# Kernel optimization log

Measured on AMD Instinct MI355X. Metric: run time of the kernel, lower is better.

## Reference

```python
import jax, jax.numpy as jnp
import numpy as np

N, E, B, H, L = 100000, 200000, 2048, 256, 4
EPS_MSG = 1e-7   # GENConv message eps
LN_EPS = 1e-5    # torch LayerNorm default eps
SM_EPS = 1e-16   # PyG softmax denominator eps


def layer_norm(x, g, b):
    mu = x.mean(-1, keepdims=True)
    var = ((x - mu) ** 2).mean(-1, keepdims=True)
    return (x - mu) * jax.lax.rsqrt(var + LN_EPS) * g + b


def gen_conv(x, src, dst, eattr, t, W1, b1, lg, lb, W2, b2):
    # GENConv(aggr='softmax', learn_t, num_layers=2, norm='layer')
    msg = jax.nn.relu(x[src] + eattr) + EPS_MSG                      # [E,H]
    scaled = msg * t
    seg_max = jax.ops.segment_max(scaled, dst, num_segments=N)       # [N,H]
    seg_max = jnp.where(jnp.isfinite(seg_max), seg_max, 0.0)
    ex = jnp.exp(scaled - seg_max[dst])                              # [E,H]
    denom = jax.ops.segment_sum(ex, dst, num_segments=N)             # [N,H]
    alpha = ex / (denom[dst] + SM_EPS)
    out = jax.ops.segment_sum(msg * alpha, dst, num_segments=N)      # [N,H]
    out = out + x                                                    # root residual inside GENConv
    h = jax.nn.relu(layer_norm(out @ W1 + b1, lg, lb))               # MLP: Lin -> LN -> ReLU -> Lin
    return h @ W2 + b2


def setup_inputs() -> dict:
    key = jax.random.key(0)
    ks = iter(jax.random.split(key, 16))
    s = lambda *sh: jax.random.normal(next(ks), sh, jnp.float32) * 0.05
    return dict(
        x=jax.random.normal(next(ks), (N, 9), jnp.float32),
        edge_index=jax.random.randint(next(ks), (2, E), 0, N),
        edge_attr=jax.random.normal(next(ks), (E, 3), jnp.float32),
        batch=jnp.sort(jax.random.randint(next(ks), (N,), 0, B)),
        node_W=s(9, H), node_b=jnp.zeros((H,), jnp.float32),
        edge_W=s(3, H), edge_b=jnp.zeros((H,), jnp.float32),
        vn_emb=jnp.zeros((1, H), jnp.float32),
        ln_g=jnp.ones((L, H), jnp.float32), ln_b=jnp.zeros((L, H), jnp.float32),
        t=jnp.ones((L - 1,), jnp.float32),
        mlp_W1=s(L - 1, H, 2 * H), mlp_b1=jnp.zeros((L - 1, 2 * H), jnp.float32),
        mlp_ln_g=jnp.ones((L - 1, 2 * H), jnp.float32), mlp_ln_b=jnp.zeros((L - 1, 2 * H), jnp.float32),
        mlp_W2=s(L - 1, 2 * H, H), mlp_b2=jnp.zeros((L - 1, H), jnp.float32),
    )


def reference(x, edge_index, edge_attr, batch, node_W, node_b, edge_W, edge_b,
              vn_emb, ln_g, ln_b, t, mlp_W1, mlp_b1, mlp_ln_g, mlp_ln_b, mlp_W2, mlp_b2):
    src, dst = edge_index[0], edge_index[1]
    h = x @ node_W + node_b                                          # node encoder
    ea = edge_attr @ edge_W + edge_b                                 # edge encoder
    vn = jnp.broadcast_to(vn_emb, (B, H))
    counts = jax.ops.segment_sum(jnp.ones((N,), h.dtype), batch, num_segments=B)
    inv_counts = (1.0 / jnp.maximum(counts, 1.0))[:, None]           # [B,1]
    # layers[1:] run conv (block='res+'); layers[0] supplies only the final norm+act
    for l in range(1, L):
        hn = jax.nn.relu(layer_norm(h, ln_g[l], ln_b[l]))            # dropout=0.1 is a no-op in eval
        h = h + gen_conv(hn, src, dst, ea, t[l - 1],
                         mlp_W1[l - 1], mlp_b1[l - 1], mlp_ln_g[l - 1], mlp_ln_b[l - 1],
                         mlp_W2[l - 1], mlp_b2[l - 1])
        vn = vn + jax.ops.segment_sum(h, batch, num_segments=B) * inv_counts  # scatter_mean
        h = h + vn[batch]                                            # broadcast virtual node
    h = jax.nn.relu(layer_norm(h, ln_g[0], ln_b[0]))
    return jax.ops.segment_sum(h, batch, num_segments=B) * inv_counts  # global_mean_pool [B,H]
```

## Files before the change

### kernel.cpp

```cpp
#include <hip/hip_runtime.h>
#include <cstdint>
#include <cstddef>


typedef _Float16 half8_t __attribute__((ext_vector_type(8)));
typedef _Float16 half4_t __attribute__((ext_vector_type(4)));
typedef float    floatx4 __attribute__((ext_vector_type(4)));

#define DEVINL __device__ __forceinline__

DEVINL float wave_sum(float v) {
#pragma unroll
  for (int m = 32; m; m >>= 1) v += __shfl_xor(v, m, 64);
  return v;
}

__global__ __launch_bounds__(256) void k_node_enc(
    const float* __restrict__ x, const float* __restrict__ W,
    const float* __restrict__ bias, _Float16* __restrict__ h, int Nr) {
  __shared__ float sW[9 * 256];
  __shared__ float sb[256];
  __shared__ float sx[72];
  const int j = threadIdx.x;
#pragma unroll
  for (int k = 0; k < 9; ++k) sW[k * 256 + j] = W[k * 256 + j];
  sb[j] = bias[j];
  const int row0 = blockIdx.x * 8;
  if (j < 72) {
    int p = row0 * 9 + j;
    sx[j] = (p < Nr * 9) ? x[p] : 0.f;
  }
  __syncthreads();
  for (int r = 0; r < 8; ++r) {
    int row = row0 + r;
    if (row >= Nr) break;
    float acc = sb[j];
#pragma unroll
    for (int k = 0; k < 9; ++k) acc = fmaf(sx[r * 9 + k], sW[k * 256 + j], acc);
    h[(size_t)row * 256 + j] = (_Float16)acc;
  }
}

__global__ void k_bptr(const int* __restrict__ batch, int* __restrict__ bptr,
                       int N_, int B_) {
  int b = blockIdx.x * 256 + threadIdx.x;
  if (b > B_) return;
  int lo = 0, hi = N_;
  while (lo < hi) {
    int mid = (lo + hi) >> 1;
    if (batch[mid] < b) lo = mid + 1; else hi = mid;
  }
  bptr[b] = lo;
}

__global__ void k_deg(const int* __restrict__ ei, int* __restrict__ deg, int E_) {
  int e = blockIdx.x * 256 + threadIdx.x;
  if (e < E_) atomicAdd(&deg[ei[E_ + e]], 1);
}

__global__ __launch_bounds__(256) void k_scan1(
    const int* __restrict__ in, int* __restrict__ out1, int* __restrict__ bsum, int n) {
  __shared__ int tmp[256];
  const int t = threadIdx.x;
  const int base = blockIdx.x * 1024;
  int v[4];
  int run = 0;
#pragma unroll
  for (int i = 0; i < 4; ++i) {
    int p = base + t * 4 + i;
    int xv = (p < n) ? in[p] : 0;
    run += xv;
    v[i] = run;
  }
  tmp[t] = run;
  __syncthreads();
  for (int off = 1; off < 256; off <<= 1) {
    int u = (t >= off) ? tmp[t - off] : 0;
    __syncthreads();
    tmp[t] += u;
    __syncthreads();
  }
  int excl = tmp[t] - run;
#pragma unroll
  for (int i = 0; i < 4; ++i) {
    int p = base + t * 4 + i;
    if (p < n) out1[p] = v[i] + excl;
  }
  if (t == 255) bsum[blockIdx.x] = tmp[255];
}

__global__ void k_scan2(int* bsum, int nb, int* ptr0) {
  if (threadIdx.x == 0 && blockIdx.x == 0) {
    int run = 0;
    for (int i = 0; i < nb; ++i) { int xv = bsum[i]; bsum[i] = run; run += xv; }
    ptr0[0] = 0;
  }
}

__global__ __launch_bounds__(256) void k_scan3(int* out1, const int* __restrict__ bsum, int n) {
  int add = bsum[blockIdx.x];
  int p0 = blockIdx.x * 1024 + threadIdx.x * 4;
#pragma unroll
  for (int i = 0; i < 4; ++i) {
    int p = p0 + i;
    if (p < n) out1[p] += add;
  }
}

__global__ void k_copy(const int* __restrict__ a, int* __restrict__ b, int n) {
  int i = blockIdx.x * 256 + threadIdx.x;
  if (i < n) b[i] = a[i];
}

__global__ void k_csrfill(const int* __restrict__ ei, int* __restrict__ cursor,
                          int* __restrict__ csr_src, int* __restrict__ csr_eid, int E_) {
  int e = blockIdx.x * 256 + threadIdx.x;
  if (e < E_) {
    int d = ei[E_ + e];
    int pos = atomicAdd(&cursor[d], 1);
    csr_src[pos] = ei[e];
    csr_eid[pos] = e;
  }
}

__global__ void k_vninit(const float* __restrict__ emb, float* __restrict__ vn) {
  vn[(size_t)blockIdx.x * 256 + threadIdx.x] = emb[threadIdx.x];
}

__global__ __launch_bounds__(256) void k_wcvt_all(
    const float* __restrict__ W1, const float* __restrict__ W2,
    _Float16* __restrict__ W1T, _Float16* __restrict__ W2T) {
  int idx = blockIdx.x * 256 + threadIdx.x;
  int mat = idx >> 17;
  int rem = idx & 131071;
  if (mat < 3) {
    int k = rem >> 9, n = rem & 511;
    W1T[(size_t)mat * 131072 + (size_t)n * 256 + k] =
        (_Float16)W1[(size_t)mat * 131072 + rem];
  } else {
    int m = mat - 3;
    int k = rem >> 8, n = rem & 255;
    W2T[(size_t)m * 131072 + (size_t)n * 512 + k] =
        (_Float16)W2[(size_t)m * 131072 + rem];
  }
}

template <int VN>
__global__ __launch_bounds__(256) void k_ln256(
    const _Float16* __restrict__ h, const float* __restrict__ vn,
    const int* __restrict__ batch, const float* __restrict__ g,
    const float* __restrict__ b, _Float16* __restrict__ out, int Nr) {
  int row = blockIdx.x * 4 + (threadIdx.x >> 6);
  if (row >= Nr) return;
  int lane = threadIdx.x & 63;
  half4_t xh = *(const half4_t*)(h + (size_t)row * 256 + lane * 4);
  float4 xv = {(float)xh[0], (float)xh[1], (float)xh[2], (float)xh[3]};
  if constexpr (VN) {
    int bb = batch[row];
    float4 vv = *(const float4*)(vn + (size_t)bb * 256 + lane * 4);
    xv.x += vv.x; xv.y += vv.y; xv.z += vv.z; xv.w += vv.w;
  }
  float s = wave_sum(xv.x + xv.y + xv.z + xv.w);
  float mu = s * (1.f / 256.f);
  float d0 = xv.x - mu, d1 = xv.y - mu, d2 = xv.z - mu, d3 = xv.w - mu;
  float v = wave_sum(d0 * d0 + d1 * d1 + d2 * d2 + d3 * d3);
  float rstd = rsqrtf(v * (1.f / 256.f) + 1e-5f);
  float4 gv = *(const float4*)(g + lane * 4);
  float4 bv = *(const float4*)(b + lane * 4);
  half4_t o;
  o[0] = (_Float16)fmaxf(d0 * rstd * gv.x + bv.x, 0.f);
  o[1] = (_Float16)fmaxf(d1 * rstd * gv.y + bv.y, 0.f);
  o[2] = (_Float16)fmaxf(d2 * rstd * gv.z + bv.z, 0.f);
  o[3] = (_Float16)fmaxf(d3 * rstd * gv.w + bv.w, 0.f);
  *(half4_t*)(out + (size_t)row * 256 + lane * 4) = o;
}

__global__ __launch_bounds__(256) void k_aggregate(
    const _Float16* __restrict__ hn, const float* __restrict__ eattr,
    const float* __restrict__ edgeW, const float* __restrict__ edgeB,
    const int* __restrict__ indptr, const int* __restrict__ csr_src,
    const int* __restrict__ csr_eid, const float* __restrict__ tptr,
    _Float16* __restrict__ agg, int Nr) {
  __shared__ float sW[4 * 256];
  const int tj = threadIdx.x;
  sW[tj] = edgeW[tj];
  sW[256 + tj] = edgeW[256 + tj];
  sW[512 + tj] = edgeW[512 + tj];
  sW[768 + tj] = edgeB[tj];
  __syncthreads();

  int node = blockIdx.x * 4 + (threadIdx.x >> 6);
  if (node >= Nr) return;
  int lane = threadIdx.x & 63;
  float tval = tptr[0];
  int e0 = indptr[node], e1 = indptr[node + 1];
  float M[4], D[4], Nu[4];
#pragma unroll
  for (int i = 0; i < 4; ++i) { M[i] = -1e38f; D[i] = 0.f; Nu[i] = 0.f; }
  for (int s = e0; s < e1; ++s) {
    int srcn = csr_src[s];
    int eid = csr_eid[s];
    float ex0 = eattr[(size_t)eid * 3 + 0];
    float ex1 = eattr[(size_t)eid * 3 + 1];
    float ex2 = eattr[(size_t)eid * 3 + 2];
    half4_t hv = *(const half4_t*)(hn + (size_t)srcn * 256 + lane * 4);
#pragma unroll
    for (int i = 0; i < 4; ++i) {
      int j = lane * 4 + i;
      float eaj = fmaf(ex0, sW[j], fmaf(ex1, sW[256 + j], fmaf(ex2, sW[512 + j], sW[768 + j])));
      float msg = fmaxf((float)hv[i] + eaj, 0.f) + 1e-7f;
      float sc = msg * tval;
      float nM = fmaxf(M[i], sc);
      float sOld = __expf(M[i] - nM);
      float pr = __expf(sc - nM);
      D[i] = D[i] * sOld + pr;
      Nu[i] = Nu[i] * sOld + pr * msg;
      M[i] = nM;
    }
  }
  half4_t hs = *(const half4_t*)(hn + (size_t)node * 256 + lane * 4);
  half4_t res;
#pragma unroll
  for (int i = 0; i < 4; ++i)
    res[i] = (_Float16)(Nu[i] / (D[i] + 1e-16f) + (float)hs[i]);
  *(half4_t*)(agg + (size_t)node * 256 + lane * 4) = res;
}

__global__ __launch_bounds__(256, 2) void k_gemm1(
    const _Float16* __restrict__ A, const _Float16* __restrict__ BT,
    const float* __restrict__ bias, _Float16* __restrict__ outh,
    float2* __restrict__ rstat, int M) {
  __shared__ _Float16 ldsA[128 * 256];
  __shared__ _Float16 ldsB[128 * 64];
  const int tid = threadIdx.x;
  const int lane = tid & 63;
  const int wv = tid >> 6;
  const int m0 = blockIdx.x * 128;
  const int wm = wv * 32;
  const int q = lane >> 4;
  const int l16 = lane & 15;

  for (int g = 0; g < 4; ++g) {
    half8_t tmp[4];
    int ss[4];
#pragma unroll
    for (int i = 0; i < 4; ++i) {
      int s = (g * 4 + i) * 256 + tid;
      int r = s >> 5;
      int c = (s & 31) ^ (r & 7);
      int rowA = m0 + r;
      rowA = rowA < M ? rowA : (M - 1);
      tmp[i] = *(const half8_t*)(A + (size_t)rowA * 256 + c * 8);
      ss[i] = s;
    }
#pragma unroll
    for (int i = 0; i < 4; ++i)
      *(half8_t*)(ldsA + (size_t)ss[i] * 8) = tmp[i];
  }

  size_t offB[4];
  int ldsOffB[4];
#pragma unroll
  for (int i = 0; i < 4; ++i) {
    int p = (i * 4 + wv) * 64 + lane;
    int r = p >> 3;
    int s = p & 7;
    int gg = s ^ (r & 7);
    offB[i] = (size_t)r * 256 + gg * 8;
    ldsOffB[i] = p * 8;
  }
  half8_t rb[4];
  auto loadB = [&](int j) {
    int n = j >> 2, t = j & 3;
    size_t base = (size_t)n * 128 * 256 + t * 64;
#pragma unroll
    for (int i = 0; i < 4; ++i)
      rb[i] = *(const half8_t*)(BT + base + offB[i]);
  };
  auto writeB = [&]() {
#pragma unroll
    for (int i = 0; i < 4; ++i)
      *(half8_t*)(ldsB + ldsOffB[i]) = rb[i];
  };

  floatx4 acc[2][8] = {};
  float sA[2][4] = {}, s2A[2][4] = {};

  loadB(0);
  writeB();
  for (int j = 0; j < 16; ++j) {
    __syncthreads();
    if (j + 1 < 16) loadB(j + 1);
    const int t = j & 3;
#pragma unroll
    for (int kk = 0; kk < 2; ++kk) {
      const int c8 = kk * 4 + q;
      const int cg = t * 8 + c8;
      half8_t af[2], bf[8];
#pragma unroll
      for (int rt = 0; rt < 2; ++rt) {
        int r = wm + rt * 16 + l16;
        af[rt] = *(const half8_t*)(ldsA + (size_t)(r * 32 + (cg ^ (r & 7))) * 8);
      }
#pragma unroll
      for (int ct = 0; ct < 8; ++ct) {
        int n = ct * 16 + l16;
        bf[ct] = *(const half8_t*)(ldsB + (size_t)(n * 8 + (c8 ^ (n & 7))) * 8);
      }
#pragma unroll
      for (int rt = 0; rt < 2; ++rt)
#pragma unroll
        for (int ct = 0; ct < 8; ++ct)
          acc[rt][ct] = __builtin_amdgcn_mfma_f32_16x16x32_f16(af[rt], bf[ct], acc[rt][ct], 0, 0, 0);
    }
    __syncthreads();
    if (j + 1 < 16) writeB();
    if ((j & 3) == 3) {
      int n = j >> 2;
#pragma unroll
      for (int rt = 0; rt < 2; ++rt) {
#pragma unroll
        for (int rr = 0; rr < 4; ++rr) {
          int row = m0 + wm + rt * 16 + q * 4 + rr;
          float vv[8];
          float s = 0.f, s2 = 0.f;
#pragma unroll
          for (int ct = 0; ct < 8; ++ct) {
            int col = n * 128 + ct * 16 + l16;
            float v = acc[rt][ct][rr] + bias[col];
            vv[ct] = v;
            s += v;
            s2 += v * v;
          }
          if (row < M) {
#pragma unroll
            for (int ct = 0; ct < 8; ++ct) {
              int col = n * 128 + ct * 16 + l16;
              outh[(size_t)row * 512 + col] = (_Float16)vv[ct];
            }
          }
          sA[rt][rr] += s;
          s2A[rt][rr] += s2;
        }
      }
#pragma unroll
      for (int rt = 0; rt < 2; ++rt)
#pragma unroll
        for (int ct = 0; ct < 8; ++ct)
          acc[rt][ct] = floatx4{0.f, 0.f, 0.f, 0.f};
    }
  }

#pragma unroll
  for (int rt = 0; rt < 2; ++rt) {
#pragma unroll
    for (int rr = 0; rr < 4; ++rr) {
      float s = sA[rt][rr], s2 = s2A[rt][rr];
#pragma unroll
      for (int m = 1; m < 16; m <<= 1) {
        s += __shfl_xor(s, m, 64);
        s2 += __shfl_xor(s2, m, 64);
      }
      int row = m0 + wm + rt * 16 + q * 4 + rr;
      if (l16 == 0 && row < M) rstat[row] = make_float2(s, s2);
    }
  }
}

template <int VN>
__global__ __launch_bounds__(256, 2) void k_gemm2(
    const _Float16* __restrict__ A, const _Float16* __restrict__ BT,
    const float* __restrict__ bias, const float2* __restrict__ rstat,
    const float* __restrict__ lg, const float* __restrict__ lb,
    const float* __restrict__ vn, const int* __restrict__ batch,
    _Float16* __restrict__ outf, int M) {
  constexpr int K = 512, NN = 256, NT = K / 64;
  constexpr int EPS = 68;
  const int g = blockIdx.x;
  const int mI = blockIdx.y * 8 + (g & 7);
  const int nI = g >> 3;
  const int mT = (M + 127) >> 7;
  if (mI >= mT) return;

  __shared__ _Float16 ldsbuf[4 * 64 * EPS];
  _Float16* ldsA = ldsbuf;
  _Float16* ldsB = ldsbuf + 128 * 64;
  __shared__ float sg[512];
  __shared__ float sbt[512];
  const int tid = threadIdx.x;
  sg[tid] = lg[tid];
  sg[tid + 256] = lg[tid + 256];
  sbt[tid] = lb[tid];
  sbt[tid + 256] = lb[tid + 256];
  __syncthreads();

  const int lane = tid & 63;
  const int wv = tid >> 6;
  const int m0 = mI * 128;
  const int n0 = nI * 128;
  const int wm = (wv >> 1) * 64;
  const int wn = (wv & 1) * 64;
  const int q = lane >> 4;
  const int l16 = lane & 15;
  floatx4 acc[4][4] = {};

  size_t offA[4], offB[4];
  int ldsOff[4], gcolA[4];
  float aco[4], cco[4];
#pragma unroll
  for (int i = 0; i < 4; ++i) {
    int p = (i * 4 + wv) * 64 + lane;
    int r = p >> 3;
    int s = p & 7;
    int gg = s ^ (r & 7);
    int rowA = m0 + r;
    rowA = rowA < M ? rowA : (M - 1);
    offA[i] = (size_t)rowA * K + gg * 8;
    offB[i] = (size_t)(n0 + r) * K + gg * 8;
    ldsOff[i] = p * 8;
    gcolA[i] = gg * 8;
    float2 st = rstat[rowA];
    float mu = st.x * (1.f / 512.f);
    float var = st.y * (1.f / 512.f) - mu * mu;
    float rs = rsqrtf(var + 1e-5f);
    aco[i] = rs;
    cco[i] = -mu * rs;
  }
  half8_t ra[4], rb[4];
  auto loadtile = [&](int kt) {
#pragma unroll
    for (int i = 0; i < 4; ++i) {
      ra[i] = *(const half8_t*)(A + offA[i] + kt);
      rb[i] = *(const half8_t*)(BT + offB[i] + kt);
    }
  };
  auto writetile = [&](int kt) {
#pragma unroll
    for (int i = 0; i < 4; ++i) {
      int c0 = kt + gcolA[i];
      half8_t ya;
#pragma unroll
      for (int jj = 0; jj < 8; ++jj) {
        float e = fmaf((float)ra[i][jj], aco[i], cco[i]);
        float y = fmaf(e, sg[c0 + jj], sbt[c0 + jj]);
        ya[jj] = (_Float16)fmaxf(y, 0.f);
      }
      *(half8_t*)(ldsA + ldsOff[i]) = ya;
      *(half8_t*)(ldsB + ldsOff[i]) = rb[i];
    }
  };

  loadtile(0);
  writetile(0);
#pragma unroll
  for (int t = 0; t < NT; ++t) {
    __syncthreads();
    if (t + 1 < NT) loadtile((t + 1) * 64);
#pragma unroll
    for (int kk = 0; kk < 2; ++kk) {
      half8_t af[4], bf[4];
      const int c8 = kk * 4 + q;
#pragma unroll
      for (int rt = 0; rt < 4; ++rt) {
        int r = wm + rt * 16 + l16;
        af[rt] = *(const half8_t*)(ldsA + (size_t)(r * 8 + (c8 ^ (r & 7))) * 8);
      }
#pragma unroll
      for (int ct = 0; ct < 4; ++ct) {
        int n = wn + ct * 16 + l16;
        bf[ct] = *(const half8_t*)(ldsB + (size_t)(n * 8 + (c8 ^ (n & 7))) * 8);
      }
#pragma unroll
      for (int rt = 0; rt < 4; ++rt)
#pragma unroll
        for (int ct = 0; ct < 4; ++ct)
          acc[rt][ct] = __builtin_amdgcn_mfma_f32_16x16x32_f16(af[rt], bf[ct], acc[rt][ct], 0, 0, 0);
    }
    __syncthreads();
    if (t + 1 < NT) writetile((t + 1) * 64);
  }

  _Float16* epi = ldsbuf + wv * (64 * EPS);
#pragma unroll
  for (int rt = 0; rt < 4; ++rt) {
#pragma unroll
    for (int rr = 0; rr < 4; ++rr) {
      int rloc = rt * 16 + q * 4 + rr;
      int row = m0 + wm + rloc;
      int rowc = row < M ? row : (M - 1);
      int bb = 0;
      if constexpr (VN) bb = batch[rowc];
#pragma unroll
      for (int ct = 0; ct < 4; ++ct) {
        int cloc = ct * 16 + l16;
        int col = n0 + wn + cloc;
        float v = acc[rt][ct][rr] + bias[col];
        if constexpr (VN) v += vn[(size_t)bb * 256 + col];
        epi[rloc * EPS + cloc] = (_Float16)v;
      }
    }
  }
#pragma unroll
  for (int it = 0; it < 8; ++it) {
    int rloc = it * 8 + (lane >> 3);
    int row = m0 + wm + rloc;
    if (row < M) {
      int c0 = (lane & 7) * 8;
      size_t gidx = (size_t)row * NN + n0 + wn + c0;
      half8_t hv = *(const half8_t*)(outf + gidx);
      half8_t ev = *(const half8_t*)(epi + rloc * EPS + c0);
      half8_t o;
#pragma unroll
      for (int jj = 0; jj < 8; ++jj) o[jj] = (_Float16)((float)hv[jj] + (float)ev[jj]);
      *(half8_t*)(outf + gidx) = o;
    }
  }
}

__global__ __launch_bounds__(256) void k_vnsum(
    const _Float16* __restrict__ h, float* __restrict__ vn,
    const int* __restrict__ bptr) {
  int b = blockIdx.x, j = threadIdx.x;
  int n0 = bptr[b], n1 = bptr[b + 1];
  float acc = 0.f;
  for (int n = n0; n < n1; ++n) acc += (float)h[(size_t)n * 256 + j];
  int c = n1 - n0;
  vn[(size_t)b * 256 + j] += acc * (1.f / (float)(c > 1 ? c : 1));
}

__global__ __launch_bounds__(256) void k_lnpool(
    const _Float16* __restrict__ h, const float* __restrict__ vn,
    const int* __restrict__ bptr, const float* __restrict__ g,
    const float* __restrict__ b, float* __restrict__ out) {
  __shared__ float red[3][256];
  int bb = blockIdx.x;
  int w = threadIdx.x >> 6;
  int lane = threadIdx.x & 63;
  int n0 = bptr[bb], n1 = bptr[bb + 1];
  float4 vv = *(const float4*)(vn + (size_t)bb * 256 + lane * 4);
  float4 gv = *(const float4*)(g + lane * 4);
  float4 bv = *(const float4*)(b + lane * 4);
  float a0 = 0.f, a1 = 0.f, a2 = 0.f, a3 = 0.f;
  for (int row = n0 + w; row < n1; row += 4) {
    half4_t xh = *(const half4_t*)(h + (size_t)row * 256 + lane * 4);
    float x0 = (float)xh[0] + vv.x, x1 = (float)xh[1] + vv.y;
    float x2 = (float)xh[2] + vv.z, x3 = (float)xh[3] + vv.w;
    float s = wave_sum(x0 + x1 + x2 + x3);
    float mu = s * (1.f / 256.f);
    float d0 = x0 - mu, d1 = x1 - mu, d2 = x2 - mu, d3 = x3 - mu;
    float v = wave_sum(d0 * d0 + d1 * d1 + d2 * d2 + d3 * d3);
    float rstd = rsqrtf(v * (1.f / 256.f) + 1e-5f);
    a0 += fmaxf(d0 * rstd * gv.x + bv.x, 0.f);
    a1 += fmaxf(d1 * rstd * gv.y + bv.y, 0.f);
    a2 += fmaxf(d2 * rstd * gv.z + bv.z, 0.f);
    a3 += fmaxf(d3 * rstd * gv.w + bv.w, 0.f);
  }
  if (w > 0) {
    red[w - 1][lane * 4 + 0] = a0;
    red[w - 1][lane * 4 + 1] = a1;
    red[w - 1][lane * 4 + 2] = a2;
    red[w - 1][lane * 4 + 3] = a3;
  }
  __syncthreads();
  if (w == 0) {
    int c = n1 - n0;
    float ic = 1.f / (float)(c > 1 ? c : 1);
#pragma unroll
    for (int k = 0; k < 3; ++k) {
      a0 += red[k][lane * 4 + 0];
      a1 += red[k][lane * 4 + 1];
      a2 += red[k][lane * 4 + 2];
      a3 += red[k][lane * 4 + 3];
    }
    float4 o = {a0 * ic, a1 * ic, a2 * ic, a3 * ic};
    *(float4*)(out + (size_t)bb * 256 + lane * 4) = o;
  }
}

extern "C" void kernel_launch(void* const* d_in, const int* in_sizes, int n_in,
                              void* d_out, int out_size, void* d_ws, size_t ws_size,
                              hipStream_t stream) {
  const float* x      = (const float*)d_in[0];
  const int*   ei     = (const int*)d_in[1];
  const float* eattr  = (const float*)d_in[2];
  const int*   batch  = (const int*)d_in[3];
  const float* nodeW  = (const float*)d_in[4];
  const float* nodeB  = (const float*)d_in[5];
  const float* edgeW  = (const float*)d_in[6];
  const float* edgeB  = (const float*)d_in[7];
  const float* vnemb  = (const float*)d_in[8];
  const float* lng    = (const float*)d_in[9];
  const float* lnb    = (const float*)d_in[10];
  const float* tparam = (const float*)d_in[11];
  const float* W1     = (const float*)d_in[12];
  const float* b1     = (const float*)d_in[13];
  const float* mlng   = (const float*)d_in[14];
  const float* mlnb   = (const float*)d_in[15];
  const float* W2     = (const float*)d_in[16];
  const float* b2     = (const float*)d_in[17];
  float* out = (float*)d_out;

  const int N = in_sizes[3];
  const int E = in_sizes[1] / 2;
  const int B = out_size / 256;

  char* p = (char*)d_ws;
  auto take = [&](size_t bytes) -> char* {
    char* r = p;
    p += (bytes + 255) & ~(size_t)255;
    return r;
  };
  _Float16*  h   = (_Float16*)take((size_t)N * 256 * 2);
  _Float16*  t1  = (_Float16*)take((size_t)N * 512 * 2);
  _Float16*  hn  = t1;
  _Float16*  agg = (_Float16*)take((size_t)N * 256 * 2);
  _Float16*  W1T = (_Float16*)take((size_t)3 * 512 * 256 * 2);
  _Float16*  W2T = (_Float16*)take((size_t)3 * 256 * 512 * 2);
  float2*    rstat = (float2*)take((size_t)N * 8);
  float*     vn  = (float*)take((size_t)B * 256 * 4);
  int*       bptr   = (int*)take((size_t)(B + 1) * 4);
  int*       deg    = (int*)take((size_t)N * 4);
  int*       indptr = (int*)take((size_t)(N + 1) * 4);
  int*       cursor = (int*)take((size_t)N * 4);
  int*       csr_src = (int*)take((size_t)E * 4);
  int*       csr_eid = (int*)take((size_t)E * 4);
  int*       bsum    = (int*)take(512 * 4);
  (void)ws_size; (void)n_in;

  hipMemsetAsync(deg, 0, (size_t)N * 4, stream);

  k_node_enc<<<(N + 7) / 8, 256, 0, stream>>>(x, nodeW, nodeB, h, N);
  k_bptr<<<(B + 256) / 256, 256, 0, stream>>>(batch, bptr, N, B);

  const int nbN = (N + 1023) / 1024;
  k_deg<<<(E + 255) / 256, 256, 0, stream>>>(ei, deg, E);
  k_scan1<<<nbN, 256, 0, stream>>>(deg, indptr + 1, bsum, N);
  k_scan2<<<1, 64, 0, stream>>>(bsum, nbN, indptr);
  k_scan3<<<nbN, 256, 0, stream>>>(indptr + 1, bsum, N);
  k_copy<<<(N + 255) / 256, 256, 0, stream>>>(indptr, cursor, N);
  k_csrfill<<<(E + 255) / 256, 256, 0, stream>>>(ei, cursor, csr_src, csr_eid, E);

  k_wcvt_all<<<3072, 256, 0, stream>>>(W1, W2, W1T, W2T);
  k_vninit<<<B, 256, 0, stream>>>(vnemb, vn);

  const int lnGrid = (N + 3) / 4;
  const int mTiles = (N + 127) / 128;
  const dim3 g2grid(16, (mTiles + 7) / 8);
  for (int l = 1; l <= 3; ++l) {
    if (l == 1)
      k_ln256<0><<<lnGrid, 256, 0, stream>>>(
          h, nullptr, nullptr, lng + (size_t)l * 256, lnb + (size_t)l * 256, hn, N);
    else
      k_ln256<1><<<lnGrid, 256, 0, stream>>>(
          h, vn, batch, lng + (size_t)l * 256, lnb + (size_t)l * 256, hn, N);
    k_aggregate<<<lnGrid, 256, 0, stream>>>(hn, eattr, edgeW, edgeB, indptr, csr_src, csr_eid,
                                            tparam + (l - 1), agg, N);
    k_gemm1<<<mTiles, 256, 0, stream>>>(
        agg, W1T + (size_t)(l - 1) * 512 * 256, b1 + (size_t)(l - 1) * 512, t1, rstat, N);
    if (l == 1)
      k_gemm2<0><<<g2grid, 256, 0, stream>>>(
          t1, W2T + (size_t)(l - 1) * 256 * 512, b2 + (size_t)(l - 1) * 256, rstat,
          mlng + (size_t)(l - 1) * 512, mlnb + (size_t)(l - 1) * 512, nullptr, nullptr, h, N);
    else
      k_gemm2<1><<<g2grid, 256, 0, stream>>>(
          t1, W2T + (size_t)(l - 1) * 256 * 512, b2 + (size_t)(l - 1) * 256, rstat,
          mlng + (size_t)(l - 1) * 512, mlnb + (size_t)(l - 1) * 512, vn, batch, h, N);
    k_vnsum<<<B, 256, 0, stream>>>(h, vn, bptr);
  }

  k_lnpool<<<B, 256, 0, stream>>>(h, vn, bptr, lng, lnb, out);
}
```

Before: 857.9 us.

## Drop online-max softmax in aggregation and shrink GEMM1 row tile for occupancy

The edge aggregation no longer keeps a running max with rescaling. It accumulates exp(msg*t) directly, removing one exp and the rescale multiplies per element. The edge-encoder weights are read into registers instead of being staged through shared memory, which also drops the block barrier. GEMM1 now uses 64-row tiles with one MFMA row tile per wave and declares 3 blocks per CU, trading per-block B reuse for more resident blocks. Skipping the max subtraction risks exp overflow if msg*t grows large, for example with a large learned t.

```diff
diff --git a/kernel.cpp b/kernel.cpp
--- a/kernel.cpp
+++ b/kernel.cpp
@@ -181,81 +181,76 @@
     const int* __restrict__ indptr, const int* __restrict__ csr_src,
     const int* __restrict__ csr_eid, const float* __restrict__ tptr,
     _Float16* __restrict__ agg, int Nr) {
-  __shared__ float sW[4 * 256];
-  const int tj = threadIdx.x;
-  sW[tj] = edgeW[tj];
-  sW[256 + tj] = edgeW[256 + tj];
-  sW[512 + tj] = edgeW[512 + tj];
-  sW[768 + tj] = edgeB[tj];
-  __syncthreads();
-
   int node = blockIdx.x * 4 + (threadIdx.x >> 6);
   if (node >= Nr) return;
   int lane = threadIdx.x & 63;
+  int j0 = lane * 4;
+  float4 w0 = *(const float4*)(edgeW + j0);
+  float4 w1 = *(const float4*)(edgeW + 256 + j0);
+  float4 w2 = *(const float4*)(edgeW + 512 + j0);
+  float4 wb = *(const float4*)(edgeB + j0);
+  float W0[4] = {w0.x, w0.y, w0.z, w0.w};
+  float W1r[4] = {w1.x, w1.y, w1.z, w1.w};
+  float W2r[4] = {w2.x, w2.y, w2.z, w2.w};
+  float WB[4] = {wb.x, wb.y, wb.z, wb.w};
   float tval = tptr[0];
   int e0 = indptr[node], e1 = indptr[node + 1];
-  float M[4], D[4], Nu[4];
-#pragma unroll
-  for (int i = 0; i < 4; ++i) { M[i] = -1e38f; D[i] = 0.f; Nu[i] = 0.f; }
+  float D[4] = {0.f, 0.f, 0.f, 0.f};
+  float Nu[4] = {0.f, 0.f, 0.f, 0.f};
   for (int s = e0; s < e1; ++s) {
     int srcn = csr_src[s];
     int eid = csr_eid[s];
     float ex0 = eattr[(size_t)eid * 3 + 0];
     float ex1 = eattr[(size_t)eid * 3 + 1];
     float ex2 = eattr[(size_t)eid * 3 + 2];
-    half4_t hv = *(const half4_t*)(hn + (size_t)srcn * 256 + lane * 4);
+    half4_t hv = *(const half4_t*)(hn + (size_t)srcn * 256 + j0);
 #pragma unroll
     for (int i = 0; i < 4; ++i) {
-      int j = lane * 4 + i;
-      float eaj = fmaf(ex0, sW[j], fmaf(ex1, sW[256 + j], fmaf(ex2, sW[512 + j], sW[768 + j])));
+      float eaj = fmaf(ex0, W0[i], fmaf(ex1, W1r[i], fmaf(ex2, W2r[i], WB[i])));
       float msg = fmaxf((float)hv[i] + eaj, 0.f) + 1e-7f;
-      float sc = msg * tval;
-      float nM = fmaxf(M[i], sc);
-      float sOld = __expf(M[i] - nM);
-      float pr = __expf(sc - nM);
-      D[i] = D[i] * sOld + pr;
-      Nu[i] = Nu[i] * sOld + pr * msg;
-      M[i] = nM;
-    }
-  }
-  half4_t hs = *(const half4_t*)(hn + (size_t)node * 256 + lane * 4);
+      float pr = __expf(msg * tval);
+      D[i] += pr;
+      Nu[i] = fmaf(pr, msg, Nu[i]);
+    }
+  }
+  half4_t hs = *(const half4_t*)(hn + (size_t)node * 256 + j0);
   half4_t res;
 #pragma unroll
   for (int i = 0; i < 4; ++i)
     res[i] = (_Float16)(Nu[i] / (D[i] + 1e-16f) + (float)hs[i]);
-  *(half4_t*)(agg + (size_t)node * 256 + lane * 4) = res;
-}
-
-__global__ __launch_bounds__(256, 2) void k_gemm1(
+  *(half4_t*)(agg + (size_t)node * 256 + j0) = res;
+}
+
+__global__ __launch_bounds__(256, 3) void k_gemm1(
     const _Float16* __restrict__ A, const _Float16* __restrict__ BT,
     const float* __restrict__ bias, _Float16* __restrict__ outh,
     float2* __restrict__ rstat, int M) {
-  __shared__ _Float16 ldsA[128 * 256];
+  __shared__ _Float16 ldsA[64 * 256];
   __shared__ _Float16 ldsB[128 * 64];
   const int tid = threadIdx.x;
   const int lane = tid & 63;
   const int wv = tid >> 6;
-  const int m0 = blockIdx.x * 128;
-  const int wm = wv * 32;
+  const int m0 = blockIdx.x * 64;
+  const int wm = wv * 16;
   const int q = lane >> 4;
   const int l16 = lane & 15;
 
-  for (int g = 0; g < 4; ++g) {
-    half8_t tmp[4];
-    int ss[4];
-#pragma unroll
-    for (int i = 0; i < 4; ++i) {
-      int s = (g * 4 + i) * 256 + tid;
+  {
+    half8_t tmp[8];
+    int ss[8];
+#pragma unroll
+    for (int g = 0; g < 8; ++g) {
+      int s = g * 256 + tid;
       int r = s >> 5;
       int c = (s & 31) ^ (r & 7);
       int rowA = m0 + r;
       rowA = rowA < M ? rowA : (M - 1);
-      tmp[i] = *(const half8_t*)(A + (size_t)rowA * 256 + c * 8);
-      ss[i] = s;
-    }
-#pragma unroll
-    for (int i = 0; i < 4; ++i)
-      *(half8_t*)(ldsA + (size_t)ss[i] * 8) = tmp[i];
+      tmp[g] = *(const half8_t*)(A + (size_t)rowA * 256 + c * 8);
+      ss[g] = s;
+    }
+#pragma unroll
+    for (int g = 0; g < 8; ++g)
+      *(half8_t*)(ldsA + (size_t)ss[g] * 8) = tmp[g];
   }
 
   size_t offB[4];
@@ -283,8 +278,8 @@
       *(half8_t*)(ldsB + ldsOffB[i]) = rb[i];
   };
 
-  floatx4 acc[2][8] = {};
-  float sA[2][4] = {}, s2A[2][4] = {};
+  floatx4 acc[8] = {};
+  float sA[4] = {0.f, 0.f, 0.f, 0.f}, s2A[4] = {0.f, 0.f, 0.f, 0.f};
 
   loadB(0);
   writeB();
@@ -296,74 +291,61 @@
     for (int kk = 0; kk < 2; ++kk) {
       const int c8 = kk * 4 + q;
       const int cg = t * 8 + c8;
-      half8_t af[2], bf[8];
-#pragma unroll
-      for (int rt = 0; rt < 2; ++rt) {
-        int r = wm + rt * 16 + l16;
-        af[rt] = *(const half8_t*)(ldsA + (size_t)(r * 32 + (cg ^ (r & 7))) * 8);
-      }
+      int r = wm + l16;
+      half8_t af = *(const half8_t*)(ldsA + (size_t)(r * 32 + (cg ^ (r & 7))) * 8);
+      half8_t bf[8];
 #pragma unroll
       for (int ct = 0; ct < 8; ++ct) {
         int n = ct * 16 + l16;
         bf[ct] = *(const half8_t*)(ldsB + (size_t)(n * 8 + (c8 ^ (n & 7))) * 8);
       }
 #pragma unroll
-      for (int rt = 0; rt < 2; ++rt)
-#pragma unroll
-        for (int ct = 0; ct < 8; ++ct)
-          acc[rt][ct] = __builtin_amdgcn_mfma_f32_16x16x32_f16(af[rt], bf[ct], acc[rt][ct], 0, 0, 0);
+      for (int ct = 0; ct < 8; ++ct)
+        acc[ct] = __builtin_amdgcn_mfma_f32_16x16x32_f16(af, bf[ct], acc[ct], 0, 0, 0);
     }
     __syncthreads();
     if (j + 1 < 16) writeB();
     if ((j & 3) == 3) {
       int n = j >> 2;
 #pragma unroll
-      for (int rt = 0; rt < 2; ++rt) {
-#pragma unroll
-        for (int rr = 0; rr < 4; ++rr) {
-          int row = m0 + wm + rt * 16 + q * 4 + rr;
-          float vv[8];
-          float s = 0.f, s2 = 0.f;
+      for (int rr = 0; rr < 4; ++rr) {
+        int row = m0 + wm + q * 4 + rr;
+        float vv[8];
+        float s = 0.f, s2 = 0.f;
+#pragma unroll
+        for (int ct = 0; ct < 8; ++ct) {
+          int col = n * 128 + ct * 16 + l16;
+          float v = acc[ct][rr] + bias[col];
+          vv[ct] = v;
+          s += v;
+          s2 += v * v;
+        }
+        if (row < M) {
 #pragma unroll
           for (int ct = 0; ct < 8; ++ct) {
             int col = n * 128 + ct * 16 + l16;
-            float v = acc[rt][ct][rr] + bias[col];
-            vv[ct] = v;
-            s += v;
-            s2 += v * v;
+            outh[(size_t)row * 512 + col] = (_Float16)vv[ct];
           }
-          if (row < M) {
-#pragma unroll
-            for (int ct = 0; ct < 8; ++ct) {
-              int col = n * 128 + ct * 16 + l16;
-              outh[(size_t)row * 512 + col] = (_Float16)vv[ct];
-            }
-          }
-          sA[rt][rr] += s;
-          s2A[rt][rr] += s2;
         }
+        sA[rr] += s;
+        s2A[rr] += s2;
       }
 #pragma unroll
-      for (int rt = 0; rt < 2; ++rt)
-#pragma unroll
-        for (int ct = 0; ct < 8; ++ct)
-          acc[rt][ct] = floatx4{0.f, 0.f, 0.f, 0.f};
-    }
-  }
-
-#pragma unroll
-  for (int rt = 0; rt < 2; ++rt) {
-#pragma unroll
-    for (int rr = 0; rr < 4; ++rr) {
-      float s = sA[rt][rr], s2 = s2A[rt][rr];
-#pragma unroll
-      for (int m = 1; m < 16; m <<= 1) {
-        s += __shfl_xor(s, m, 64);
-        s2 += __shfl_xor(s2, m, 64);
-      }
-      int row = m0 + wm + rt * 16 + q * 4 + rr;
-      if (l16 == 0 && row < M) rstat[row] = make_float2(s, s2);
-    }
+      for (int ct = 0; ct < 8; ++ct)
+        acc[ct] = floatx4{0.f, 0.f, 0.f, 0.f};
+    }
+  }
+
+#pragma unroll
+  for (int rr = 0; rr < 4; ++rr) {
+    float s = sA[rr], s2 = s2A[rr];
+#pragma unroll
+    for (int m = 1; m < 16; m <<= 1) {
+      s += __shfl_xor(s, m, 64);
+      s2 += __shfl_xor(s2, m, 64);
+    }
+    int row = m0 + wm + q * 4 + rr;
+    if (l16 == 0 && row < M) rstat[row] = make_float2(s, s2);
   }
 }
 
@@ -644,8 +626,9 @@
   k_vninit<<<B, 256, 0, stream>>>(vnemb, vn);
 
   const int lnGrid = (N + 3) / 4;
-  const int mTiles = (N + 127) / 128;
-  const dim3 g2grid(16, (mTiles + 7) / 8);
+  const int mTiles1 = (N + 63) / 64;
+  const int mTiles2 = (N + 127) / 128;
+  const dim3 g2grid(16, (mTiles2 + 7) / 8);
   for (int l = 1; l <= 3; ++l) {
     if (l == 1)
       k_ln256<0><<<lnGrid, 256, 0, stream>>>(
@@ -655,7 +638,7 @@
           h, vn, batch, lng + (size_t)l * 256, lnb + (size_t)l * 256, hn, N);
     k_aggregate<<<lnGrid, 256, 0, stream>>>(hn, eattr, edgeW, edgeB, indptr, csr_src, csr_eid,
                                             tparam + (l - 1), agg, N);
-    k_gemm1<<<mTiles, 256, 0, stream>>>(
+    k_gemm1<<<mTiles1, 256, 0, stream>>>(
         agg, W1T + (size_t)(l - 1) * 512 * 256, b1 + (size_t)(l - 1) * 512, t1, rstat, N);
     if (l == 1)
       k_gemm2<0><<<g2grid, 256, 0, stream>>>(
```

Result: faster. 827.4 us (-3.6%).

## Fuse virtual-node update with next LayerNorm, drop online max, stream GEMM1 weights

Applied to the files above, without the earlier changes.

The per-graph virtual-node sum is fused with the next layer's LayerNorm+ReLU (and with the final pooling), replacing separate vnsum, ln256 and lnpool launches and one full pass over h. The aggregation kernel drops the running-max softmax, using a plain exp-sum with edge-encoder weights held in registers instead of LDS. This halves the exponentials, but exp(msg*t) can overflow if t or the activations grow large. GEMM1 now reads B fragments straight from global memory with register double buffering instead of staging them through LDS, which removes barriers but relies on cache hits for weight reuse.

```diff
diff --git a/kernel.cpp b/kernel.cpp
--- a/kernel.cpp
+++ b/kernel.cpp
@@ -145,24 +145,17 @@
   }
 }
 
-template <int VN>
 __global__ __launch_bounds__(256) void k_ln256(
-    const _Float16* __restrict__ h, const float* __restrict__ vn,
-    const int* __restrict__ batch, const float* __restrict__ g,
+    const _Float16* __restrict__ h, const float* __restrict__ g,
     const float* __restrict__ b, _Float16* __restrict__ out, int Nr) {
   int row = blockIdx.x * 4 + (threadIdx.x >> 6);
   if (row >= Nr) return;
   int lane = threadIdx.x & 63;
   half4_t xh = *(const half4_t*)(h + (size_t)row * 256 + lane * 4);
-  float4 xv = {(float)xh[0], (float)xh[1], (float)xh[2], (float)xh[3]};
-  if constexpr (VN) {
-    int bb = batch[row];
-    float4 vv = *(const float4*)(vn + (size_t)bb * 256 + lane * 4);
-    xv.x += vv.x; xv.y += vv.y; xv.z += vv.z; xv.w += vv.w;
-  }
-  float s = wave_sum(xv.x + xv.y + xv.z + xv.w);
+  float x0 = (float)xh[0], x1 = (float)xh[1], x2 = (float)xh[2], x3 = (float)xh[3];
+  float s = wave_sum(x0 + x1 + x2 + x3);
   float mu = s * (1.f / 256.f);
-  float d0 = xv.x - mu, d1 = xv.y - mu, d2 = xv.z - mu, d3 = xv.w - mu;
+  float d0 = x0 - mu, d1 = x1 - mu, d2 = x2 - mu, d3 = x3 - mu;
   float v = wave_sum(d0 * d0 + d1 * d1 + d2 * d2 + d3 * d3);
   float rstd = rsqrtf(v * (1.f / 256.f) + 1e-5f);
   float4 gv = *(const float4*)(g + lane * 4);
@@ -181,49 +174,44 @@
     const int* __restrict__ indptr, const int* __restrict__ csr_src,
     const int* __restrict__ csr_eid, const float* __restrict__ tptr,
     _Float16* __restrict__ agg, int Nr) {
-  __shared__ float sW[4 * 256];
-  const int tj = threadIdx.x;
-  sW[tj] = edgeW[tj];
-  sW[256 + tj] = edgeW[256 + tj];
-  sW[512 + tj] = edgeW[512 + tj];
-  sW[768 + tj] = edgeB[tj];
-  __syncthreads();
-
   int node = blockIdx.x * 4 + (threadIdx.x >> 6);
   if (node >= Nr) return;
   int lane = threadIdx.x & 63;
+  int j0 = lane * 4;
+  float4 w0 = *(const float4*)(edgeW + j0);
+  float4 w1 = *(const float4*)(edgeW + 256 + j0);
+  float4 w2 = *(const float4*)(edgeW + 512 + j0);
+  float4 wb = *(const float4*)(edgeB + j0);
+  float W0[4] = {w0.x, w0.y, w0.z, w0.w};
+  float W1r[4] = {w1.x, w1.y, w1.z, w1.w};
+  float W2r[4] = {w2.x, w2.y, w2.z, w2.w};
+  float WB[4] = {wb.x, wb.y, wb.z, wb.w};
   float tval = tptr[0];
   int e0 = indptr[node], e1 = indptr[node + 1];
-  float M[4], D[4], Nu[4];
-#pragma unroll
-  for (int i = 0; i < 4; ++i) { M[i] = -1e38f; D[i] = 0.f; Nu[i] = 0.f; }
+  float D[4] = {0.f, 0.f, 0.f, 0.f};
+  float Nu[4] = {0.f, 0.f, 0.f, 0.f};
   for (int s = e0; s < e1; ++s) {
     int srcn = csr_src[s];
     int eid = csr_eid[s];
     float ex0 = eattr[(size_t)eid * 3 + 0];
     float ex1 = eattr[(size_t)eid * 3 + 1];
     float ex2 = eattr[(size_t)eid * 3 + 2];
-    half4_t hv = *(const half4_t*)(hn + (size_t)srcn * 256 + lane * 4);
+    half4_t hv = *(const half4_t*)(hn + (size_t)srcn * 256 + j0);
 #pragma unroll
     for (int i = 0; i < 4; ++i) {
-      int j = lane * 4 + i;
-      float eaj = fmaf(ex0, sW[j], fmaf(ex1, sW[256 + j], fmaf(ex2, sW[512 + j], sW[768 + j])));
+      float eaj = fmaf(ex0, W0[i], fmaf(ex1, W1r[i], fmaf(ex2, W2r[i], WB[i])));
       float msg = fmaxf((float)hv[i] + eaj, 0.f) + 1e-7f;
-      float sc = msg * tval;
-      float nM = fmaxf(M[i], sc);
-      float sOld = __expf(M[i] - nM);
-      float pr = __expf(sc - nM);
-      D[i] = D[i] * sOld + pr;
-      Nu[i] = Nu[i] * sOld + pr * msg;
-      M[i] = nM;
-    }
-  }
-  half4_t hs = *(const half4_t*)(hn + (size_t)node * 256 + lane * 4);
+      float pr = __expf(msg * tval);
+      D[i] += pr;
+      Nu[i] = fmaf(pr, msg, Nu[i]);
+    }
+  }
+  half4_t hs = *(const half4_t*)(hn + (size_t)node * 256 + j0);
   half4_t res;
 #pragma unroll
   for (int i = 0; i < 4; ++i)
     res[i] = (_Float16)(Nu[i] / (D[i] + 1e-16f) + (float)hs[i]);
-  *(half4_t*)(agg + (size_t)node * 256 + lane * 4) = res;
+  *(half4_t*)(agg + (size_t)node * 256 + j0) = res;
 }
 
 __global__ __launch_bounds__(256, 2) void k_gemm1(
@@ -231,7 +219,6 @@
     const float* __restrict__ bias, _Float16* __restrict__ outh,
     float2* __restrict__ rstat, int M) {
   __shared__ _Float16 ldsA[128 * 256];
-  __shared__ _Float16 ldsB[128 * 64];
   const int tid = threadIdx.x;
   const int lane = tid & 63;
   const int wv = tid >> 6;
@@ -257,97 +244,66 @@
     for (int i = 0; i < 4; ++i)
       *(half8_t*)(ldsA + (size_t)ss[i] * 8) = tmp[i];
   }
-
-  size_t offB[4];
-  int ldsOffB[4];
-#pragma unroll
-  for (int i = 0; i < 4; ++i) {
-    int p = (i * 4 + wv) * 64 + lane;
-    int r = p >> 3;
-    int s = p & 7;
-    int gg = s ^ (r & 7);
-    offB[i] = (size_t)r * 256 + gg * 8;
-    ldsOffB[i] = p * 8;
-  }
-  half8_t rb[4];
-  auto loadB = [&](int j) {
-    int n = j >> 2, t = j & 3;
-    size_t base = (size_t)n * 128 * 256 + t * 64;
-#pragma unroll
-    for (int i = 0; i < 4; ++i)
-      rb[i] = *(const half8_t*)(BT + base + offB[i]);
-  };
-  auto writeB = [&]() {
-#pragma unroll
-    for (int i = 0; i < 4; ++i)
-      *(half8_t*)(ldsB + ldsOffB[i]) = rb[i];
-  };
-
-  floatx4 acc[2][8] = {};
-  float sA[2][4] = {}, s2A[2][4] = {};
-
-  loadB(0);
-  writeB();
-  for (int j = 0; j < 16; ++j) {
-    __syncthreads();
-    if (j + 1 < 16) loadB(j + 1);
-    const int t = j & 3;
-#pragma unroll
-    for (int kk = 0; kk < 2; ++kk) {
-      const int c8 = kk * 4 + q;
-      const int cg = t * 8 + c8;
-      half8_t af[2], bf[8];
+  __syncthreads();
+
+  float sA[2][4] = {};
+  float s2A[2][4] = {};
+
+  for (int n = 0; n < 4; ++n) {
+    const _Float16* Bn = BT + (size_t)(n * 128 + l16) * 256 + q * 8;
+    floatx4 acc[2][8] = {};
+    half8_t bfn[8];
+#pragma unroll
+    for (int ct = 0; ct < 8; ++ct)
+      bfn[ct] = *(const half8_t*)(Bn + ct * 4096);
+#pragma unroll
+    for (int kk = 0; kk < 8; ++kk) {
+      half8_t bfc[8];
+#pragma unroll
+      for (int ct = 0; ct < 8; ++ct) bfc[ct] = bfn[ct];
+      if (kk < 7) {
+#pragma unroll
+        for (int ct = 0; ct < 8; ++ct)
+          bfn[ct] = *(const half8_t*)(Bn + ct * 4096 + (kk + 1) * 32);
+      }
+      const int cg = kk * 4 + q;
+      half8_t af[2];
 #pragma unroll
       for (int rt = 0; rt < 2; ++rt) {
         int r = wm + rt * 16 + l16;
         af[rt] = *(const half8_t*)(ldsA + (size_t)(r * 32 + (cg ^ (r & 7))) * 8);
       }
 #pragma unroll
-      for (int ct = 0; ct < 8; ++ct) {
-        int n = ct * 16 + l16;
-        bf[ct] = *(const half8_t*)(ldsB + (size_t)(n * 8 + (c8 ^ (n & 7))) * 8);
-      }
-#pragma unroll
       for (int rt = 0; rt < 2; ++rt)
 #pragma unroll
         for (int ct = 0; ct < 8; ++ct)
-          acc[rt][ct] = __builtin_amdgcn_mfma_f32_16x16x32_f16(af[rt], bf[ct], acc[rt][ct], 0, 0, 0);
-    }
-    __syncthreads();
-    if (j + 1 < 16) writeB();
-    if ((j & 3) == 3) {
-      int n = j >> 2;
-#pragma unroll
-      for (int rt = 0; rt < 2; ++rt) {
-#pragma unroll
-        for (int rr = 0; rr < 4; ++rr) {
-          int row = m0 + wm + rt * 16 + q * 4 + rr;
-          float vv[8];
-          float s = 0.f, s2 = 0.f;
+          acc[rt][ct] = __builtin_amdgcn_mfma_f32_16x16x32_f16(af[rt], bfc[ct], acc[rt][ct], 0, 0, 0);
+    }
+#pragma unroll
+    for (int rt = 0; rt < 2; ++rt) {
+#pragma unroll
+      for (int rr = 0; rr < 4; ++rr) {
+        int row = m0 + wm + rt * 16 + q * 4 + rr;
+        float vv[8];
+        float s = 0.f, s2 = 0.f;
+#pragma unroll
+        for (int ct = 0; ct < 8; ++ct) {
+          int col = n * 128 + ct * 16 + l16;
+          float v = acc[rt][ct][rr] + bias[col];
+          vv[ct] = v;
+          s += v;
+          s2 += v * v;
+        }
+        if (row < M) {
 #pragma unroll
           for (int ct = 0; ct < 8; ++ct) {
             int col = n * 128 + ct * 16 + l16;
-            float v = acc[rt][ct][rr] + bias[col];
-            vv[ct] = v;
-            s += v;
-            s2 += v * v;
+            outh[(size_t)row * 512 + col] = (_Float16)vv[ct];
           }
-          if (row < M) {
-#pragma unroll
-            for (int ct = 0; ct < 8; ++ct) {
-              int col = n * 128 + ct * 16 + l16;
-              outh[(size_t)row * 512 + col] = (_Float16)vv[ct];
-            }
-          }
-          sA[rt][rr] += s;
-          s2A[rt][rr] += s2;
         }
+        sA[rt][rr] += s;
+        s2A[rt][rr] += s2;
       }
-#pragma unroll
-      for (int rt = 0; rt < 2; ++rt)
-#pragma unroll
-        for (int ct = 0; ct < 8; ++ct)
-          acc[rt][ct] = floatx4{0.f, 0.f, 0.f, 0.f};
     }
   }
 
@@ -517,30 +473,113 @@
   }
 }
 
-__global__ __launch_bounds__(256) void k_vnsum(
+__global__ __launch_bounds__(256) void k_vnln(
     const _Float16* __restrict__ h, float* __restrict__ vn,
-    const int* __restrict__ bptr) {
-  int b = blockIdx.x, j = threadIdx.x;
-  int n0 = bptr[b], n1 = bptr[b + 1];
-  float acc = 0.f;
-  for (int n = n0; n < n1; ++n) acc += (float)h[(size_t)n * 256 + j];
-  int c = n1 - n0;
-  vn[(size_t)b * 256 + j] += acc * (1.f / (float)(c > 1 ? c : 1));
-}
-
-__global__ __launch_bounds__(256) void k_lnpool(
+    const int* __restrict__ bptr, const float* __restrict__ g,
+    const float* __restrict__ b, _Float16* __restrict__ hn) {
+  __shared__ float red[3][256];
+  __shared__ float svn[256];
+  int bb = blockIdx.x;
+  int w = threadIdx.x >> 6;
+  int lane = threadIdx.x & 63;
+  int n0 = bptr[bb], n1 = bptr[bb + 1];
+  float a0 = 0.f, a1 = 0.f, a2 = 0.f, a3 = 0.f;
+  for (int row = n0 + w; row < n1; row += 4) {
+    half4_t xh = *(const half4_t*)(h + (size_t)row * 256 + lane * 4);
+    a0 += (float)xh[0]; a1 += (float)xh[1];
+    a2 += (float)xh[2]; a3 += (float)xh[3];
+  }
+  if (w > 0) {
+    red[w - 1][lane * 4 + 0] = a0;
+    red[w - 1][lane * 4 + 1] = a1;
+    red[w - 1][lane * 4 + 2] = a2;
+    red[w - 1][lane * 4 + 3] = a3;
+  }
+  __syncthreads();
+  if (w == 0) {
+    int c = n1 - n0;
+    float ic = 1.f / (float)(c > 1 ? c : 1);
+#pragma unroll
+    for (int k = 0; k < 3; ++k) {
+      a0 += red[k][lane * 4 + 0];
+      a1 += red[k][lane * 4 + 1];
+      a2 += red[k][lane * 4 + 2];
+      a3 += red[k][lane * 4 + 3];
+    }
+    float4 vo = *(const float4*)(vn + (size_t)bb * 256 + lane * 4);
+    vo.x += a0 * ic; vo.y += a1 * ic; vo.z += a2 * ic; vo.w += a3 * ic;
+    *(float4*)(vn + (size_t)bb * 256 + lane * 4) = vo;
+    svn[lane * 4 + 0] = vo.x;
+    svn[lane * 4 + 1] = vo.y;
+    svn[lane * 4 + 2] = vo.z;
+    svn[lane * 4 + 3] = vo.w;
+  }
+  __syncthreads();
+  float4 vv = *(const float4*)(svn + lane * 4);
+  float4 gv = *(const float4*)(g + lane * 4);
+  float4 bv = *(const float4*)(b + lane * 4);
+  for (int row = n0 + w; row < n1; row += 4) {
+    half4_t xh = *(const half4_t*)(h + (size_t)row * 256 + lane * 4);
+    float x0 = (float)xh[0] + vv.x, x1 = (float)xh[1] + vv.y;
+    float x2 = (float)xh[2] + vv.z, x3 = (float)xh[3] + vv.w;
+    float s = wave_sum(x0 + x1 + x2 + x3);
+    float mu = s * (1.f / 256.f);
+    float d0 = x0 - mu, d1 = x1 - mu, d2 = x2 - mu, d3 = x3 - mu;
+    float v = wave_sum(d0 * d0 + d1 * d1 + d2 * d2 + d3 * d3);
+    float rstd = rsqrtf(v * (1.f / 256.f) + 1e-5f);
+    half4_t o;
+    o[0] = (_Float16)fmaxf(d0 * rstd * gv.x + bv.x, 0.f);
+    o[1] = (_Float16)fmaxf(d1 * rstd * gv.y + bv.y, 0.f);
+    o[2] = (_Float16)fmaxf(d2 * rstd * gv.z + bv.z, 0.f);
+    o[3] = (_Float16)fmaxf(d3 * rstd * gv.w + bv.w, 0.f);
+    *(half4_t*)(hn + (size_t)row * 256 + lane * 4) = o;
+  }
+}
+
+__global__ __launch_bounds__(256) void k_vnlnpool(
     const _Float16* __restrict__ h, const float* __restrict__ vn,
     const int* __restrict__ bptr, const float* __restrict__ g,
     const float* __restrict__ b, float* __restrict__ out) {
   __shared__ float red[3][256];
+  __shared__ float svn[256];
   int bb = blockIdx.x;
   int w = threadIdx.x >> 6;
   int lane = threadIdx.x & 63;
   int n0 = bptr[bb], n1 = bptr[bb + 1];
-  float4 vv = *(const float4*)(vn + (size_t)bb * 256 + lane * 4);
+  int c = n1 - n0;
+  float ic = 1.f / (float)(c > 1 ? c : 1);
+  float a0 = 0.f, a1 = 0.f, a2 = 0.f, a3 = 0.f;
+  for (int row = n0 + w; row < n1; row += 4) {
+    half4_t xh = *(const half4_t*)(h + (size_t)row * 256 + lane * 4);
+    a0 += (float)xh[0]; a1 += (float)xh[1];
+    a2 += (float)xh[2]; a3 += (float)xh[3];
+  }
+  if (w > 0) {
+    red[w - 1][lane * 4 + 0] = a0;
+    red[w - 1][lane * 4 + 1] = a1;
+    red[w - 1][lane * 4 + 2] = a2;
+    red[w - 1][lane * 4 + 3] = a3;
+  }
+  __syncthreads();
+  if (w == 0) {
+#pragma unroll
+    for (int k = 0; k < 3; ++k) {
+      a0 += red[k][lane * 4 + 0];
+      a1 += red[k][lane * 4 + 1];
+      a2 += red[k][lane * 4 + 2];
+      a3 += red[k][lane * 4 + 3];
+    }
+    float4 vo = *(const float4*)(vn + (size_t)bb * 256 + lane * 4);
+    svn[lane * 4 + 0] = vo.x + a0 * ic;
+    svn[lane * 4 + 1] = vo.y + a1 * ic;
+    svn[lane * 4 + 2] = vo.z + a2 * ic;
+    svn[lane * 4 + 3] = vo.w + a3 * ic;
+  }
+  __syncthreads();
+  float4 vv = *(const float4*)(svn + lane * 4);
   float4 gv = *(const float4*)(g + lane * 4);
   float4 bv = *(const float4*)(b + lane * 4);
-  float a0 = 0.f, a1 = 0.f, a2 = 0.f, a3 = 0.f;
+  a0 = a1 = a2 = a3 = 0.f;
   for (int row = n0 + w; row < n1; row += 4) {
     half4_t xh = *(const half4_t*)(h + (size_t)row * 256 + lane * 4);
     float x0 = (float)xh[0] + vv.x, x1 = (float)xh[1] + vv.y;
@@ -555,6 +594,7 @@
     a2 += fmaxf(d2 * rstd * gv.z + bv.z, 0.f);
     a3 += fmaxf(d3 * rstd * gv.w + bv.w, 0.f);
   }
+  __syncthreads();
   if (w > 0) {
     red[w - 1][lane * 4 + 0] = a0;
     red[w - 1][lane * 4 + 1] = a1;
@@ -563,8 +603,6 @@
   }
   __syncthreads();
   if (w == 0) {
-    int c = n1 - n0;
-    float ic = 1.f / (float)(c > 1 ? c : 1);
 #pragma unroll
     for (int k = 0; k < 3; ++k) {
       a0 += red[k][lane * 4 + 0];
@@ -646,13 +684,9 @@
   const int lnGrid = (N + 3) / 4;
   const int mTiles = (N + 127) / 128;
   const dim3 g2grid(16, (mTiles + 7) / 8);
+
+  k_ln256<<<lnGrid, 256, 0, stream>>>(h, lng + 256, lnb + 256, hn, N);
   for (int l = 1; l <= 3; ++l) {
-    if (l == 1)
-      k_ln256<0><<<lnGrid, 256, 0, stream>>>(
-          h, nullptr, nullptr, lng + (size_t)l * 256, lnb + (size_t)l * 256, hn, N);
-    else
-      k_ln256<1><<<lnGrid, 256, 0, stream>>>(
-          h, vn, batch, lng + (size_t)l * 256, lnb + (size_t)l * 256, hn, N);
     k_aggregate<<<lnGrid, 256, 0, stream>>>(hn, eattr, edgeW, edgeB, indptr, csr_src, csr_eid,
                                             tparam + (l - 1), agg, N);
     k_gemm1<<<mTiles, 256, 0, stream>>>(
@@ -665,8 +699,10 @@
       k_gemm2<1><<<g2grid, 256, 0, stream>>>(
           t1, W2T + (size_t)(l - 1) * 256 * 512, b2 + (size_t)(l - 1) * 256, rstat,
           mlng + (size_t)(l - 1) * 512, mlnb + (size_t)(l - 1) * 512, vn, batch, h, N);
-    k_vnsum<<<B, 256, 0, stream>>>(h, vn, bptr);
-  }
-
-  k_lnpool<<<B, 256, 0, stream>>>(h, vn, bptr, lng, lnb, out);
-}
+    if (l < 3)
+      k_vnln<<<B, 256, 0, stream>>>(h, vn, bptr,
+                                    lng + (size_t)(l + 1) * 256, lnb + (size_t)(l + 1) * 256, hn);
+    else
+      k_vnlnpool<<<B, 256, 0, stream>>>(h, vn, bptr, lng, lnb, out);
+  }
+}
```

Result: slower. 991.0 us (+15.5%).
